# Performance work log

Measured on AMD Instinct MI355X. Metric: run time of the kernel, lower is better.

## Reference

```python
import jax, jax.numpy as jnp
import numpy as np
from jax import lax

SCALE = 128.0        # x/y/w/h scale = model input size
MIN_SCORE = 0.5      # min_score_thresh
IOU_THRESH = 0.3     # mediapipe min_suppression_threshold
MAX_DET = 64         # fixed detection slots (jit-safe replacement for dynamic list)
NUM_ANCHORS = 896


def _decode(raw_boxes, anchors):
    # raw_boxes [B,A,16], anchors [A,4] = (x_center, y_center, w, h)
    ax, ay, aw, ah = anchors[:, 0], anchors[:, 1], anchors[:, 2], anchors[:, 3]
    xc = raw_boxes[..., 0] / SCALE * aw + ax
    yc = raw_boxes[..., 1] / SCALE * ah + ay
    w = raw_boxes[..., 2] / SCALE * aw
    h = raw_boxes[..., 3] / SCALE * ah
    box = jnp.stack([yc - h / 2, xc - w / 2, yc + h / 2, xc + w / 2], axis=-1)  # [B,A,4] ymin,xmin,ymax,xmax
    kp = raw_boxes[..., 4:16].reshape(*raw_boxes.shape[:-1], 6, 2)  # [B,A,6,2] (x,y)
    kpx = kp[..., 0] / SCALE * aw[:, None] + ax[:, None]
    kpy = kp[..., 1] / SCALE * ah[:, None] + ay[:, None]
    kps = jnp.stack([kpx, kpy], axis=-1).reshape(*raw_boxes.shape[:-1], 12)
    return jnp.concatenate([box, kps], axis=-1)  # [B,A,16]


def _iou(box, boxes):
    # box [4], boxes [A,4]; coords = ymin,xmin,ymax,xmax
    ymin = jnp.maximum(box[0], boxes[:, 0])
    xmin = jnp.maximum(box[1], boxes[:, 1])
    ymax = jnp.minimum(box[2], boxes[:, 2])
    xmax = jnp.minimum(box[3], boxes[:, 3])
    inter = jnp.maximum(ymax - ymin, 0.0) * jnp.maximum(xmax - xmin, 0.0)
    a1 = jnp.maximum(box[2] - box[0], 0.0) * jnp.maximum(box[3] - box[1], 0.0)
    a2 = jnp.maximum(boxes[:, 2] - boxes[:, 0], 0.0) * jnp.maximum(boxes[:, 3] - boxes[:, 1], 0.0)
    return inter / jnp.maximum(a1 + a2 - inter, 1e-6)


def _weighted_nms_single(coords, scores):
    # coords [A,16], scores [A] -> out [MAX_DET,17] sorted by descending score, zero-padded
    rem = jnp.where(scores >= MIN_SCORE, scores, -1.0)

    def step(rem, _):
        idx = jnp.argmax(rem)
        best = rem[idx]
        iou = _iou(coords[idx, :4], coords[:, :4])
        overlap = (iou > IOU_THRESH) & (rem > 0.0)
        wts = jnp.where(overlap, scores, 0.0)            # weight = candidate score
        denom = jnp.maximum(wts.sum(), 1e-6)
        blended = (coords * wts[:, None]).sum(0) / denom  # weighted box + keypoints
        det = jnp.concatenate([blended, best[None]])
        det = jnp.where(best > 0.0, det, jnp.zeros(17, det.dtype))
        rem = jnp.where(overlap, -1.0, rem)
        return rem, det

    _, out = lax.scan(step, rem, None, length=MAX_DET)
    return out


def _project(dets, matrix):
    # dets [B,MAX_DET,17], matrix [B,8] (first two rows of row-major 4x4 affine)
    m = matrix[:, None, :]  # [B,1,8]
    x_idx = jnp.array([1, 3, 4, 6, 8, 10, 12, 14])
    y_idx = jnp.array([0, 2, 5, 7, 9, 11, 13, 15])
    xs = dets[..., x_idx]
    ys = dets[..., y_idx]
    new_x = xs * m[..., 0:1] + ys * m[..., 1:2] + m[..., 3:4]
    new_y = xs * m[..., 4:5] + ys * m[..., 5:6] + m[..., 7:8]
    out = dets.at[..., x_idx].set(new_x)
    out = out.at[..., y_idx].set(new_y)
    # keep padded (invalid) rows zero, like the segmented-tensor original
    valid = dets[..., 16:17] > 0.0
    return jnp.where(valid, out, 0.0)


def _rescale(dets, h, w):
    hf = jnp.float32(h)
    wf = jnp.float32(w)
    scale = jnp.concatenate([
        jnp.array([1.0, 1.0]) * 0 + jnp.stack([hf, wf]),   # ymin*h, xmin*w
        jnp.stack([hf, wf]),                               # ymax*h, xmax*w
        jnp.tile(jnp.stack([wf, hf]), 6),                  # kp x*w, kp y*h
        jnp.ones((1,), jnp.float32),                       # score unchanged
    ])
    return dets * scale


def setup_inputs() -> dict:
    key = jax.random.key(0)
    k1, k2, k3, k4 = jax.random.split(key, 4)
    B = 2048
    return {
        "raw_boxes": jax.random.normal(k1, (B, NUM_ANCHORS, 16), jnp.float32),
        "raw_scores": jax.random.normal(k2, (B, NUM_ANCHORS), jnp.float32),
        "anchors": jax.random.uniform(k3, (NUM_ANCHORS, 4), jnp.float32),
        "transform_matrix": jax.random.normal(k4, (B, 8), jnp.float32),
        "h": 720,
        "w": 1280,
    }


def reference(raw_boxes, raw_scores, anchors, transform_matrix, h, w):
    coords = _decode(raw_boxes, anchors)                       # [B,A,16]
    scores = jax.nn.sigmoid(jnp.clip(raw_scores, -100.0, 100.0))
    dets = jax.vmap(_weighted_nms_single)(coords, scores)      # [B,MAX_DET,17]
    dets = _project(dets, transform_matrix)
    dets = _rescale(dets, h, w)
    return dets
```

## Files before the change

### kernel.cpp

```cpp
#include <hip/hip_runtime.h>
#include <math.h>

#define NANCH 896
#define MAXD 64
#define MAXSLOTS 14

__device__ __forceinline__ float selv17(const float d[17], int c) {
    float v = d[0];
#pragma unroll
    for (int k = 1; k < 17; ++k) v = (c == k) ? d[k] : v;
    return v;
}

__global__ __launch_bounds__(256, 2) void blaze_kernel(
    const float* __restrict__ raw_boxes,
    const float* __restrict__ raw_scores,
    const float* __restrict__ anchors,
    const float* __restrict__ tmat,
    const int* __restrict__ hptr,
    const int* __restrict__ wptr,
    float* __restrict__ out)
{
    __shared__ float scoords[NANCH * 16];
    __shared__ float sscore[NANCH];
    __shared__ int   wcnt[16];
    __shared__ float sdet[17];

    const int b    = blockIdx.x;
    const int tid  = threadIdx.x;
    const int lane = tid & 63;
    const int wv   = tid >> 6;

    const float* rb = raw_boxes  + (size_t)b * (NANCH * 16);
    const float* rs = raw_scores + (size_t)b * NANCH;

    float sval[4];
    bool  act[4];
#pragma unroll
    for (int r = 0; r < 4; ++r) {
        int a = r * 256 + tid;
        float s = -1.f;
        if (a < NANCH) {
            float x = rs[a];
            x = fminf(fmaxf(x, -100.f), 100.f);
            s = 1.f / (1.f + expf(-x));
        }
        sval[r] = s;
        act[r]  = (s >= 0.5f);
    }
    unsigned long long bm[4];
#pragma unroll
    for (int r = 0; r < 4; ++r) {
        bm[r] = __ballot(act[r]);
        if (lane == 0) wcnt[r * 4 + wv] = __popcll(bm[r]);
    }
    __syncthreads();
    int pos[4];
    int base = 0;
#pragma unroll
    for (int r = 0; r < 4; ++r) {
        int off = base;
        for (int w2 = 0; w2 < wv; ++w2) off += wcnt[r * 4 + w2];
        pos[r] = off + (int)__popcll(bm[r] & ((1ull << lane) - 1ull));
        base += wcnt[r * 4 + 0] + wcnt[r * 4 + 1] + wcnt[r * 4 + 2] + wcnt[r * 4 + 3];
    }
    const int count = base;

#pragma unroll
    for (int r = 0; r < 4; ++r) {
        int a = r * 256 + tid;
        if (act[r]) {
            float4 an = *(const float4*)(anchors + a * 4);
            float4 r0 = *(const float4*)(rb + a * 16);
            float4 r1 = *(const float4*)(rb + a * 16 + 4);
            float4 r2 = *(const float4*)(rb + a * 16 + 8);
            float4 r3 = *(const float4*)(rb + a * 16 + 12);
            float ax = an.x, ay = an.y, aw = an.z, ah = an.w;
            const float inv = 1.f / 128.f;
            float xc = r0.x * inv * aw + ax;
            float yc = r0.y * inv * ah + ay;
            float ww = r0.z * inv * aw;
            float hh = r0.w * inv * ah;
            float4* dst = (float4*)(scoords + pos[r] * 16);
            dst[0] = make_float4(yc - hh * 0.5f, xc - ww * 0.5f,
                                 yc + hh * 0.5f, xc + ww * 0.5f);
            dst[1] = make_float4(r1.x * inv * aw + ax, r1.y * inv * ah + ay,
                                 r1.z * inv * aw + ax, r1.w * inv * ah + ay);
            dst[2] = make_float4(r2.x * inv * aw + ax, r2.y * inv * ah + ay,
                                 r2.z * inv * aw + ax, r2.w * inv * ah + ay);
            dst[3] = make_float4(r3.x * inv * aw + ax, r3.y * inv * ah + ay,
                                 r3.z * inv * aw + ax, r3.w * inv * ah + ay);
            sscore[pos[r]] = sval[r];
        }
    }
    __syncthreads();

    if (wv != 0) return;

    float rem[MAXSLOTS];
#pragma unroll
    for (int j = 0; j < MAXSLOTS; ++j) {
        int i = lane + 64 * j;
        float v = -1.f;
        if (i < count) v = sscore[i];
        rem[j] = v;
    }

    const float* M = tmat + (size_t)b * 8;
    const float m0 = M[0], m1 = M[1], m3 = M[3];
    const float m4 = M[4], m5 = M[5], m7 = M[7];
    const float hf = (float)(*hptr);
    const float wf = (float)(*wptr);
    float* ob = out + (size_t)b * (MAXD * 17);

    int iter = 0;
    while (true) {
        float bv = -2.f; int bi = 1 << 30;
#pragma unroll
        for (int j = 0; j < MAXSLOTS; ++j) {
            if (64 * j < count) {
                if (rem[j] > bv) { bv = rem[j]; bi = lane + 64 * j; }
            }
        }
#pragma unroll
        for (int s2 = 32; s2 >= 1; s2 >>= 1) {
            float ov = __shfl_xor(bv, s2, 64);
            int   oi = __shfl_xor(bi, s2, 64);
            if (ov > bv || (ov == bv && oi < bi)) { bv = ov; bi = oi; }
        }

        if (bv <= 0.f) {
            int n = (MAXD - iter) * 17;
            float* op = ob + iter * 17;
            for (int e = lane; e < n; e += 64) op[e] = 0.f;
            break;
        }

        float4 bb = *(const float4*)(scoords + bi * 16);
        float a1 = fmaxf(bb.z - bb.x, 0.f) * fmaxf(bb.w - bb.y, 0.f);

        float acc[16];
#pragma unroll
        for (int c = 0; c < 16; ++c) acc[c] = 0.f;
        float wsum = 0.f;
        bool anyov = false;

#pragma unroll
        for (int j = 0; j < MAXSLOTS; ++j) {
            if (64 * j < count) {
                int i = lane + 64 * j;
                bool valid = (i < count) && (rem[j] > 0.f);
                if (valid) {
                    const float4* cp = (const float4*)(scoords + i * 16);
                    float4 c0 = cp[0];
                    float ai = fmaxf(c0.z - c0.x, 0.f) * fmaxf(c0.w - c0.y, 0.f);
                    float yA = fmaxf(bb.x, c0.x);
                    float xA = fmaxf(bb.y, c0.y);
                    float yB = fminf(bb.z, c0.z);
                    float xB = fminf(bb.w, c0.w);
                    float inter = fmaxf(yB - yA, 0.f) * fmaxf(xB - xA, 0.f);
                    float iou = inter / fmaxf(a1 + ai - inter, 1e-6f);
                    if (iou > 0.3f) {
                        anyov = true;
                        float wj = sscore[i];
                        rem[j] = -1.f;
                        wsum += wj;
                        float4 c1 = cp[1], c2 = cp[2], c3 = cp[3];
                        acc[0]  += c0.x * wj; acc[1]  += c0.y * wj;
                        acc[2]  += c0.z * wj; acc[3]  += c0.w * wj;
                        acc[4]  += c1.x * wj; acc[5]  += c1.y * wj;
                        acc[6]  += c1.z * wj; acc[7]  += c1.w * wj;
                        acc[8]  += c2.x * wj; acc[9]  += c2.y * wj;
                        acc[10] += c2.z * wj; acc[11] += c2.w * wj;
                        acc[12] += c3.x * wj; acc[13] += c3.y * wj;
                        acc[14] += c3.z * wj; acc[15] += c3.w * wj;
                    }
                }
            }
        }

        bool stuck = (__ballot(anyov) == 0ull);

        float det[17];
        if (!stuck) {
#pragma unroll
            for (int s2 = 32; s2 >= 1; s2 >>= 1) {
                wsum += __shfl_xor(wsum, s2, 64);
#pragma unroll
                for (int c = 0; c < 16; ++c) acc[c] += __shfl_xor(acc[c], s2, 64);
            }
            float dnm = fmaxf(wsum, 1e-6f);
#pragma unroll
            for (int c = 0; c < 16; ++c) det[c] = acc[c] / dnm;
        } else {
#pragma unroll
            for (int c = 0; c < 16; ++c) det[c] = 0.f;
        }
        det[16] = bv;

        {
            const int xi[8] = { 1, 3, 4, 6, 8, 10, 12, 14 };
            const int yi[8] = { 0, 2, 5, 7, 9, 11, 13, 15 };
#pragma unroll
            for (int k = 0; k < 8; ++k) {
                float x = det[xi[k]], y = det[yi[k]];
                det[xi[k]] = (x * m0 + y * m1 + m3) * wf;
                det[yi[k]] = (x * m4 + y * m5 + m7) * hf;
            }
        }

        if (stuck) {
            if (lane < 17) sdet[lane] = selv17(det, lane);
            int n = (MAXD - iter) * 17;
            float* op = ob + iter * 17;
            for (int e = lane; e < n; e += 64) {
                int c = e % 17;
                op[e] = sdet[c];
            }
            break;
        } else {
            if (lane < 17) ob[iter * 17 + lane] = selv17(det, lane);
            ++iter;
            if (iter == MAXD) break;
        }
    }
}

extern "C" void kernel_launch(void* const* d_in, const int* in_sizes, int n_in,
                              void* d_out, int out_size, void* d_ws, size_t ws_size,
                              hipStream_t stream) {
    (void)n_in; (void)out_size; (void)d_ws; (void)ws_size;
    const float* raw_boxes  = (const float*)d_in[0];
    const float* raw_scores = (const float*)d_in[1];
    const float* anchors    = (const float*)d_in[2];
    const float* tmat       = (const float*)d_in[3];
    const int*   hptr       = (const int*)d_in[4];
    const int*   wptr       = (const int*)d_in[5];
    float* out = (float*)d_out;

    const int B = in_sizes[0] / (NANCH * 16);
    blaze_kernel<<<B, 256, 0, stream>>>(raw_boxes, raw_scores, anchors, tmat,
                                        hptr, wptr, out);
}
```

Measured before the change: 219.2 us.

## Store only boxes in LDS and decode keypoints lazily from global memory

New measurement: 203.1 us. -7.4%, faster.

```diff
diff --git a/kernel.cpp b/kernel.cpp
--- a/kernel.cpp
+++ b/kernel.cpp
@@ -12,7 +12,7 @@
     return v;
 }
 
-__global__ __launch_bounds__(256, 2) void blaze_kernel(
+__global__ __launch_bounds__(256, 5) void blaze_kernel(
     const float* __restrict__ raw_boxes,
     const float* __restrict__ raw_scores,
     const float* __restrict__ anchors,
@@ -21,10 +21,11 @@
     const int* __restrict__ wptr,
     float* __restrict__ out)
 {
-    __shared__ float scoords[NANCH * 16];
-    __shared__ float sscore[NANCH];
-    __shared__ int   wcnt[16];
-    __shared__ float sdet[17];
+    __shared__ float4 sbox[NANCH];
+    __shared__ float  sscore[NANCH];
+    __shared__ int    sidx[NANCH];
+    __shared__ int    wcnt[16];
+    __shared__ float  sdet[17];
 
     const int b    = blockIdx.x;
     const int tid  = threadIdx.x;
@@ -33,6 +34,7 @@
 
     const float* rb = raw_boxes  + (size_t)b * (NANCH * 16);
     const float* rs = raw_scores + (size_t)b * NANCH;
+    const float inv = 1.f / 128.f;
 
     float sval[4];
     bool  act[4];
@@ -72,25 +74,14 @@
         if (act[r]) {
             float4 an = *(const float4*)(anchors + a * 4);
             float4 r0 = *(const float4*)(rb + a * 16);
-            float4 r1 = *(const float4*)(rb + a * 16 + 4);
-            float4 r2 = *(const float4*)(rb + a * 16 + 8);
-            float4 r3 = *(const float4*)(rb + a * 16 + 12);
-            float ax = an.x, ay = an.y, aw = an.z, ah = an.w;
-            const float inv = 1.f / 128.f;
-            float xc = r0.x * inv * aw + ax;
-            float yc = r0.y * inv * ah + ay;
-            float ww = r0.z * inv * aw;
-            float hh = r0.w * inv * ah;
-            float4* dst = (float4*)(scoords + pos[r] * 16);
-            dst[0] = make_float4(yc - hh * 0.5f, xc - ww * 0.5f,
-                                 yc + hh * 0.5f, xc + ww * 0.5f);
-            dst[1] = make_float4(r1.x * inv * aw + ax, r1.y * inv * ah + ay,
-                                 r1.z * inv * aw + ax, r1.w * inv * ah + ay);
-            dst[2] = make_float4(r2.x * inv * aw + ax, r2.y * inv * ah + ay,
-                                 r2.z * inv * aw + ax, r2.w * inv * ah + ay);
-            dst[3] = make_float4(r3.x * inv * aw + ax, r3.y * inv * ah + ay,
-                                 r3.z * inv * aw + ax, r3.w * inv * ah + ay);
+            float xc = r0.x * inv * an.z + an.x;
+            float yc = r0.y * inv * an.w + an.y;
+            float ww = r0.z * inv * an.z;
+            float hh = r0.w * inv * an.w;
+            sbox[pos[r]] = make_float4(yc - hh * 0.5f, xc - ww * 0.5f,
+                                       yc + hh * 0.5f, xc + ww * 0.5f);
             sscore[pos[r]] = sval[r];
+            sidx[pos[r]]   = a;
         }
     }
     __syncthreads();
@@ -101,9 +92,7 @@
 #pragma unroll
     for (int j = 0; j < MAXSLOTS; ++j) {
         int i = lane + 64 * j;
-        float v = -1.f;
-        if (i < count) v = sscore[i];
-        rem[j] = v;
+        rem[j] = (i < count) ? sscore[i] : -1.f;
     }
 
     const float* M = tmat + (size_t)b * 8;
@@ -136,7 +125,7 @@
             break;
         }
 
-        float4 bb = *(const float4*)(scoords + bi * 16);
+        float4 bb = sbox[bi];
         float a1 = fmaxf(bb.z - bb.x, 0.f) * fmaxf(bb.w - bb.y, 0.f);
 
         float acc[16];
@@ -151,8 +140,7 @@
                 int i = lane + 64 * j;
                 bool valid = (i < count) && (rem[j] > 0.f);
                 if (valid) {
-                    const float4* cp = (const float4*)(scoords + i * 16);
-                    float4 c0 = cp[0];
+                    float4 c0 = sbox[i];
                     float ai = fmaxf(c0.z - c0.x, 0.f) * fmaxf(c0.w - c0.y, 0.f);
                     float yA = fmaxf(bb.x, c0.x);
                     float xA = fmaxf(bb.y, c0.y);
@@ -165,15 +153,26 @@
                         float wj = sscore[i];
                         rem[j] = -1.f;
                         wsum += wj;
-                        float4 c1 = cp[1], c2 = cp[2], c3 = cp[3];
-                        acc[0]  += c0.x * wj; acc[1]  += c0.y * wj;
-                        acc[2]  += c0.z * wj; acc[3]  += c0.w * wj;
-                        acc[4]  += c1.x * wj; acc[5]  += c1.y * wj;
-                        acc[6]  += c1.z * wj; acc[7]  += c1.w * wj;
-                        acc[8]  += c2.x * wj; acc[9]  += c2.y * wj;
-                        acc[10] += c2.z * wj; acc[11] += c2.w * wj;
-                        acc[12] += c3.x * wj; acc[13] += c3.y * wj;
-                        acc[14] += c3.z * wj; acc[15] += c3.w * wj;
+                        acc[0] += c0.x * wj; acc[1] += c0.y * wj;
+                        acc[2] += c0.z * wj; acc[3] += c0.w * wj;
+                        int a = sidx[i];
+                        float4 an = *(const float4*)(anchors + a * 4);
+                        const float* rp = rb + a * 16;
+                        float4 r1 = *(const float4*)(rp + 4);
+                        float4 r2 = *(const float4*)(rp + 8);
+                        float4 r3 = *(const float4*)(rp + 12);
+                        acc[4]  += (r1.x * inv * an.z + an.x) * wj;
+                        acc[5]  += (r1.y * inv * an.w + an.y) * wj;
+                        acc[6]  += (r1.z * inv * an.z + an.x) * wj;
+                        acc[7]  += (r1.w * inv * an.w + an.y) * wj;
+                        acc[8]  += (r2.x * inv * an.z + an.x) * wj;
+                        acc[9]  += (r2.y * inv * an.w + an.y) * wj;
+                        acc[10] += (r2.z * inv * an.z + an.x) * wj;
+                        acc[11] += (r2.w * inv * an.w + an.y) * wj;
+                        acc[12] += (r3.x * inv * an.z + an.x) * wj;
+                        acc[13] += (r3.y * inv * an.w + an.y) * wj;
+                        acc[14] += (r3.z * inv * an.z + an.x) * wj;
+                        acc[15] += (r3.w * inv * an.w + an.y) * wj;
                     }
                 }
             }
```
